# Optimization experiments

Measured on AMD Instinct MI355X. Metric: run time of the kernel, lower is better.

Reference implementation:

```python
import jax, jax.numpy as jnp
import numpy as np

B, D, N, P, MAXG, K = 1024, 128, 131072, 64, 2048, 16


def _l2norm(x, eps=1e-12):
    # matches torch F.normalize: x / clamp_min(||x||, eps)
    return x / jnp.maximum(jnp.linalg.norm(x, axis=-1, keepdims=True), eps)


def setup_inputs() -> dict:
    key = jax.random.key(0)
    ks = jax.random.split(key, 7)
    query = jax.random.normal(ks[0], (B, D), jnp.float32)
    keys = jax.random.normal(ks[1], (N, D), jnp.float32)
    vals = jax.random.normal(ks[2], (N, D), jnp.float32)
    labels = jax.random.normal(ks[3], (N,), jnp.float32)
    hard_assignment = jax.random.randint(ks[4], (B,), 0, P)
    cached_groups = jax.random.randint(ks[5], (P, MAXG), 0, N)
    group_sizes = jax.random.randint(ks[6], (P,), K, MAXG + 1)
    # -1 padding beyond each group's size, as in cache_sample_groups
    pos = jnp.arange(MAXG)[None, :]
    cached_groups = jnp.where(pos < group_sizes[:, None], cached_groups, -1)
    return dict(query=query, keys=keys, vals=vals, labels=labels,
                hard_assignment=hard_assignment, cached_groups=cached_groups,
                group_sizes=group_sizes, k=K)


def reference(query, keys, vals, labels, hard_assignment, cached_groups, group_sizes, k):
    n = keys.shape[0]
    q_norm = _l2norm(query)                                  # (B, D)
    grp = group_sizes[hard_assignment]                       # (B,)
    normal = grp >= k                                        # fallback mask (grp<k -> zeros)
    cand = cached_groups[hard_assignment]                    # (B, G) padded with -1
    valid = cand >= 0
    safe = jnp.clip(cand, 0, n - 1)
    keys_c = _l2norm(keys[safe])                             # (B, G, D) gathered + normalized
    sim = jnp.einsum('bd,bgd->bg', q_norm, keys_c)           # cosine similarity
    sim = jnp.where(valid, sim, -1e9)                        # mask padded candidates
    _, top = jax.lax.top_k(sim, k)                           # (B, k) positions within group
    i_final = jnp.take_along_axis(safe, top, axis=1)         # (B, k) memory-bank indices
    nk = keys[i_final]                                       # (B, k, D)
    nv = vals[i_final]                                       # (B, k, D)
    nl = labels[jnp.clip(i_final, 0, n - 1)]                 # (B, k)
    m = normal[:, None]
    nk = jnp.where(m[..., None], nk, 0.0)
    nv = jnp.where(m[..., None], nv, 0.0)
    nl = jnp.where(m, nl, 0.0)
    top_k_idx = jnp.where(m, i_final, 0)
    return nk, nv, nl, top_k_idx
```

## Files before the change

### kernel.cpp

```cpp
#include <hip/hip_runtime.h>

#define DIMS 128
#define KTOP 16
#define SMAX 2048
#define SLICE 64
#define CK 64
#define QT 32
#define CQ 32
#define NTHR 256

__device__ __forceinline__ unsigned long long packsim(float v, int g) {
    unsigned u = __float_as_uint(v);
    u = (u & 0x80000000u) ? ~u : (u | 0x80000000u);
    return ((unsigned long long)u << 32) | (unsigned)(0xFFFFFFFFu - (unsigned)g);
}

__global__ __launch_bounds__(1024)
void bucket_kernel(const int* __restrict__ hard_assign,
                   int* __restrict__ qcount, int* __restrict__ qlist, int B, int P)
{
    const int t = threadIdx.x;
    for (int i = t; i < P; i += 1024) qcount[i] = 0;
    __syncthreads();
    for (int b = t; b < B; b += 1024) {
        const int p = hard_assign[b];
        const int slot = atomicAdd(&qcount[p], 1);
        qlist[(size_t)p * B + slot] = b;
    }
}

__global__ __launch_bounds__(NTHR)
void score_kernel(const float* __restrict__ query,
                  const float* __restrict__ keys,
                  const int*   __restrict__ cached_groups,
                  const int*   __restrict__ qcount,
                  const int*   __restrict__ qlist,
                  float* __restrict__ sims,
                  int B, int N, int MAXG, int nslice)
{
    __shared__ float s_keyT[DIMS * CK];
    __shared__ float s_qT[DIMS * CQ];
    __shared__ float s_inv[SLICE];
    __shared__ int   s_g[SLICE];
    __shared__ int   s_qb[QT];

    const int p = blockIdx.x / nslice;
    const int s = blockIdx.x % nslice;
    const int cnt = qcount[p];
    if (cnt == 0) return;

    const int t = threadIdx.x;
    const int base = s * SLICE;
    const int* gp = cached_groups + (size_t)p * MAXG;
    const int* ql = qlist + (size_t)p * B;

    if (t < 128) {
        const int r    = t >> 1;
        const int half = t & 1;
        const int cand = (base + r < MAXG) ? gp[base + r] : -1;
        if (half == 0) s_g[r] = cand;
        const int sf = cand < 0 ? 0 : (cand > N - 1 ? N - 1 : cand);
        const float* kr = keys + (size_t)sf * DIMS + half * 64;
        float4 v[16];
        #pragma unroll
        for (int i = 0; i < 16; ++i)
            v[i] = *(const float4*)(kr + i * 4);
        float ks = 0.0f;
        #pragma unroll
        for (int i = 0; i < 16; ++i) {
            const int d = half * 64 + i * 4;
            ks += v[i].x * v[i].x + v[i].y * v[i].y
                + v[i].z * v[i].z + v[i].w * v[i].w;
            s_keyT[(d + 0) * CK + r] = v[i].x;
            s_keyT[(d + 1) * CK + r] = v[i].y;
            s_keyT[(d + 2) * CK + r] = v[i].z;
            s_keyT[(d + 3) * CK + r] = v[i].w;
        }
        ks += __shfl_xor(ks, 1, 64);
        if (half == 0) s_inv[r] = 1.0f / fmaxf(sqrtf(ks), 1e-12f);
    } else {
        const int tq   = t - 128;
        const int q    = tq & 31;
        const int dblk = tq >> 5;
        const int sq   = ql[(q < cnt) ? q : (cnt - 1)];
        if (dblk == 0) s_qb[q] = sq;
        const float* qr = query + (size_t)sq * DIMS + dblk * 32;
        #pragma unroll
        for (int i = 0; i < 8; ++i) {
            const float4 v = *(const float4*)(qr + i * 4);
            const int d = dblk * 32 + i * 4;
            s_qT[(d + 0) * CQ + q] = v.x;
            s_qT[(d + 1) * CQ + q] = v.y;
            s_qT[(d + 2) * CQ + q] = v.z;
            s_qT[(d + 3) * CQ + q] = v.w;
        }
    }
    __syncthreads();

    const int q0 = (t >> 4) * 2;
    const int c0 = (t & 15) * 4;

    for (int qbase = 0; ; ) {
        float acc[2][4];
        #pragma unroll
        for (int a = 0; a < 2; ++a)
            #pragma unroll
            for (int bb = 0; bb < 4; ++bb) acc[a][bb] = 0.0f;

        #pragma unroll 8
        for (int k = 0; k < DIMS; ++k) {
            const float2 aq = *(const float2*)&s_qT[k * CQ + q0];
            const float4 bk = *(const float4*)&s_keyT[k * CK + c0];
            acc[0][0] += aq.x * bk.x; acc[0][1] += aq.x * bk.y;
            acc[0][2] += aq.x * bk.z; acc[0][3] += aq.x * bk.w;
            acc[1][0] += aq.y * bk.x; acc[1][1] += aq.y * bk.y;
            acc[1][2] += aq.y * bk.z; acc[1][3] += aq.y * bk.w;
        }

        const float4 inv = *(const float4*)&s_inv[c0];
        const int4   gv  = *(const int4*)&s_g[c0];
        #pragma unroll
        for (int qi = 0; qi < 2; ++qi) {
            const int ii = qbase + q0 + qi;
            if (ii < cnt) {
                const int b = s_qb[q0 + qi];
                float4 o;
                o.x = (gv.x >= 0) ? acc[qi][0] * inv.x : -1.0e9f;
                o.y = (gv.y >= 0) ? acc[qi][1] * inv.y : -1.0e9f;
                o.z = (gv.z >= 0) ? acc[qi][2] * inv.z : -1.0e9f;
                o.w = (gv.w >= 0) ? acc[qi][3] * inv.w : -1.0e9f;
                float* dst = sims + (size_t)b * MAXG + base + c0;
                if (base + c0 + 3 < MAXG) {
                    *(float4*)dst = o;
                } else {
                    if (base + c0 + 0 < MAXG) dst[0] = o.x;
                    if (base + c0 + 1 < MAXG) dst[1] = o.y;
                    if (base + c0 + 2 < MAXG) dst[2] = o.z;
                }
            }
        }

        qbase += QT;
        if (qbase >= cnt) break;

        __syncthreads();
        if (t >= 128) {
            const int tq   = t - 128;
            const int q    = tq & 31;
            const int dblk = tq >> 5;
            const int ii   = qbase + q;
            const int sq   = ql[(ii < cnt) ? ii : (cnt - 1)];
            if (dblk == 0) s_qb[q] = sq;
            const float* qr = query + (size_t)sq * DIMS + dblk * 32;
            #pragma unroll
            for (int i = 0; i < 8; ++i) {
                const float4 v = *(const float4*)(qr + i * 4);
                const int d = dblk * 32 + i * 4;
                s_qT[(d + 0) * CQ + q] = v.x;
                s_qT[(d + 1) * CQ + q] = v.y;
                s_qT[(d + 2) * CQ + q] = v.z;
                s_qT[(d + 3) * CQ + q] = v.w;
            }
        }
        __syncthreads();
    }
}

#define CASW(x,y) { if ((x) < (y)) { const unsigned long long _t = (x); (x) = (y); (y) = _t; } }

__global__ __launch_bounds__(256)
void topk_gather_kernel(const float* __restrict__ keys,
                        const float* __restrict__ vals,
                        const float* __restrict__ labels,
                        const int*   __restrict__ hard_assign,
                        const int*   __restrict__ cached_groups,
                        const int*   __restrict__ group_sizes,
                        const float* __restrict__ sims,
                        float* __restrict__ out,
                        int B, int MAXG)
{
    const int b = blockIdx.x, t = threadIdx.x;
    const int lane = t & 63, w = t >> 6;
    const int sub = t & 15, cg = t >> 4;

    __shared__ unsigned long long s_merge[64];
    __shared__ int s_wing[KTOP];

    const int p = hard_assign[b];
    const int grpsz = group_sizes[p];
    const bool normal = (grpsz >= KTOP);
    const int* gptr = cached_groups + (size_t)p * MAXG;
    const float* simrow = sims + (size_t)b * MAXG;

    unsigned long long k0, k1, k2, k3, k4, k5, k6, k7;
    {
        const int g0 = w * (SMAX / 4) + lane * 8;
        if (g0 + 7 < MAXG) {
            const float4 va = *(const float4*)(simrow + g0);
            const float4 vb = *(const float4*)(simrow + g0 + 4);
            k0 = packsim(va.x, g0 + 0); k1 = packsim(va.y, g0 + 1);
            k2 = packsim(va.z, g0 + 2); k3 = packsim(va.w, g0 + 3);
            k4 = packsim(vb.x, g0 + 4); k5 = packsim(vb.y, g0 + 5);
            k6 = packsim(vb.z, g0 + 6); k7 = packsim(vb.w, g0 + 7);
        } else {
            #define LDK(j) packsim((g0 + (j) < MAXG) ? simrow[g0 + (j)] : -3.0e38f, g0 + (j))
            k0 = LDK(0); k1 = LDK(1); k2 = LDK(2); k3 = LDK(3);
            k4 = LDK(4); k5 = LDK(5); k6 = LDK(6); k7 = LDK(7);
            #undef LDK
        }
    }
    CASW(k0,k1) CASW(k2,k3) CASW(k4,k5) CASW(k6,k7)
    CASW(k0,k2) CASW(k1,k3) CASW(k4,k6) CASW(k5,k7)
    CASW(k1,k2) CASW(k5,k6)
    CASW(k0,k4) CASW(k1,k5) CASW(k2,k6) CASW(k3,k7)
    CASW(k2,k4) CASW(k3,k5)
    CASW(k1,k2) CASW(k3,k4) CASW(k5,k6)

    #pragma unroll 1
    for (int r = 0; r < KTOP; ++r) {
        unsigned long long wm = k0;
        #pragma unroll
        for (int off = 1; off < 64; off <<= 1) {
            const unsigned long long o = __shfl_xor(wm, off, 64);
            wm = (o > wm) ? o : wm;
        }
        if (lane == 0) s_merge[w * KTOP + r] = wm;
        if (k0 == wm) {
            k0 = k1; k1 = k2; k2 = k3; k3 = k4;
            k4 = k5; k5 = k6; k6 = k7; k7 = 0ull;
        }
    }
    __syncthreads();

    if (w == 0) {
        unsigned long long u = s_merge[lane];
        #pragma unroll
        for (int k = 2; k <= 64; k <<= 1) {
            #pragma unroll
            for (int j = k >> 1; j > 0; j >>= 1) {
                const unsigned long long o = __shfl_xor(u, j, 64);
                const bool low = (lane & j) == 0;
                const bool asc = (lane & k) == 0;
                const unsigned long long mn = (u < o) ? u : o;
                const unsigned long long mx = (u < o) ? o : u;
                u = (low == asc) ? mn : mx;
            }
        }
        if (lane >= 64 - KTOP)
            s_wing[63 - lane] = (int)(0xFFFFFFFFu - (unsigned)(u & 0xFFFFFFFFull));
    }
    __syncthreads();

    const int g    = s_wing[cg];
    const int cand = gptr[g];
    const int idx  = cand < 0 ? 0 : cand;

    const size_t BK = (size_t)B * KTOP;
    float* out_nk = out;
    float* out_nv = out + BK * DIMS;
    float* out_nl = out + 2 * BK * DIMS;
    float* out_id = out_nl + BK;

    const size_t od = ((size_t)b * KTOP + cg) * DIMS + sub * 8;
    if (normal) {
        const float* kr = keys + (size_t)idx * DIMS + sub * 8;
        const float* vr = vals + (size_t)idx * DIMS + sub * 8;
        *(float4*)(out_nk + od)     = *(const float4*)(kr);
        *(float4*)(out_nk + od + 4) = *(const float4*)(kr + 4);
        *(float4*)(out_nv + od)     = *(const float4*)(vr);
        *(float4*)(out_nv + od + 4) = *(const float4*)(vr + 4);
        if (sub == 0) {
            out_nl[(size_t)b * KTOP + cg] = labels[idx];
            out_id[(size_t)b * KTOP + cg] = (float)idx;
        }
    } else {
        const float4 z = make_float4(0.f, 0.f, 0.f, 0.f);
        *(float4*)(out_nk + od)     = z;
        *(float4*)(out_nk + od + 4) = z;
        *(float4*)(out_nv + od)     = z;
        *(float4*)(out_nv + od + 4) = z;
        if (sub == 0) {
            out_nl[(size_t)b * KTOP + cg] = 0.0f;
            out_id[(size_t)b * KTOP + cg] = 0.0f;
        }
    }
}

extern "C" void kernel_launch(void* const* d_in, const int* in_sizes, int n_in,
                              void* d_out, int out_size, void* d_ws, size_t ws_size,
                              hipStream_t stream) {
    const float* query  = (const float*)d_in[0];
    const float* keys   = (const float*)d_in[1];
    const float* vals   = (const float*)d_in[2];
    const float* labels = (const float*)d_in[3];
    const int* hard_assign   = (const int*)d_in[4];
    const int* cached_groups = (const int*)d_in[5];
    const int* group_sizes   = (const int*)d_in[6];

    const int B = in_sizes[0] / DIMS;
    const int N = in_sizes[1] / DIMS;
    const int P = in_sizes[6];
    const int MAXG = in_sizes[5] / P;
    const int nslice = (MAXG + SLICE - 1) / SLICE;

    float* sims  = (float*)d_ws;
    int* qcount  = (int*)((char*)d_ws + (size_t)B * MAXG * 4);
    int* qlist   = qcount + P;

    bucket_kernel<<<1, 1024, 0, stream>>>(hard_assign, qcount, qlist, B, P);

    score_kernel<<<P * nslice, NTHR, 0, stream>>>(
        query, keys, cached_groups, qcount, qlist, sims, B, N, MAXG, nslice);

    topk_gather_kernel<<<B, 256, 0, stream>>>(
        keys, vals, labels, hard_assign, cached_groups, group_sizes, sims,
        (float*)d_out, B, MAXG);
}
```

Before: 50.36 us.

## Process two key slices per block with register prefetch of second slice

```diff
diff --git a/kernel.cpp b/kernel.cpp
--- a/kernel.cpp
+++ b/kernel.cpp
@@ -36,7 +36,7 @@
                   const int*   __restrict__ qcount,
                   const int*   __restrict__ qlist,
                   float* __restrict__ sims,
-                  int B, int N, int MAXG, int nslice)
+                  int B, int N, int MAXG, int nslice, int npair)
 {
     __shared__ float s_keyT[DIMS * CK];
     __shared__ float s_qT[DIMS * CQ];
@@ -44,20 +44,28 @@
     __shared__ int   s_g[SLICE];
     __shared__ int   s_qb[QT];
 
-    const int p = blockIdx.x / nslice;
-    const int s = blockIdx.x % nslice;
+    const int p  = blockIdx.x / npair;
+    const int pr = blockIdx.x % npair;
+    const int s0 = pr * 2;
+    const int s1 = s0 + 1;
     const int cnt = qcount[p];
     if (cnt == 0) return;
 
     const int t = threadIdx.x;
-    const int base = s * SLICE;
+    const int base0 = s0 * SLICE;
+    const int base1 = s1 * SLICE;
+    const bool have1 = (s1 < nslice);
     const int* gp = cached_groups + (size_t)p * MAXG;
     const int* ql = qlist + (size_t)p * B;
 
+    const int r    = t >> 1;
+    const int half = t & 1;
+
+    int cand1 = -1;
+    if (t < 128 && have1 && base1 + r < MAXG) cand1 = gp[base1 + r];
+
     if (t < 128) {
-        const int r    = t >> 1;
-        const int half = t & 1;
-        const int cand = (base + r < MAXG) ? gp[base + r] : -1;
+        const int cand = (base0 + r < MAXG) ? gp[base0 + r] : -1;
         if (half == 0) s_g[r] = cand;
         const int sf = cand < 0 ? 0 : (cand > N - 1 ? N - 1 : cand);
         const float* kr = keys + (size_t)sf * DIMS + half * 64;
@@ -97,73 +105,128 @@
     }
     __syncthreads();
 
+    float4 pv[16];
+    {
+        const int sf1 = cand1 < 0 ? 0 : (cand1 > N - 1 ? N - 1 : cand1);
+        if (t < 128 && have1) {
+            const float* kr1 = keys + (size_t)sf1 * DIMS + half * 64;
+            #pragma unroll
+            for (int i = 0; i < 16; ++i)
+                pv[i] = *(const float4*)(kr1 + i * 4);
+        }
+    }
+    asm volatile("" ::: "memory");
+
     const int q0 = (t >> 4) * 2;
     const int c0 = (t & 15) * 4;
 
-    for (int qbase = 0; ; ) {
-        float acc[2][4];
-        #pragma unroll
-        for (int a = 0; a < 2; ++a)
+    auto compute_slice = [&](const int base) {
+        for (int qbase = 0; ; ) {
+            float acc[2][4];
             #pragma unroll
-            for (int bb = 0; bb < 4; ++bb) acc[a][bb] = 0.0f;
-
-        #pragma unroll 8
-        for (int k = 0; k < DIMS; ++k) {
-            const float2 aq = *(const float2*)&s_qT[k * CQ + q0];
-            const float4 bk = *(const float4*)&s_keyT[k * CK + c0];
-            acc[0][0] += aq.x * bk.x; acc[0][1] += aq.x * bk.y;
-            acc[0][2] += aq.x * bk.z; acc[0][3] += aq.x * bk.w;
-            acc[1][0] += aq.y * bk.x; acc[1][1] += aq.y * bk.y;
-            acc[1][2] += aq.y * bk.z; acc[1][3] += aq.y * bk.w;
-        }
-
-        const float4 inv = *(const float4*)&s_inv[c0];
-        const int4   gv  = *(const int4*)&s_g[c0];
-        #pragma unroll
-        for (int qi = 0; qi < 2; ++qi) {
-            const int ii = qbase + q0 + qi;
-            if (ii < cnt) {
-                const int b = s_qb[q0 + qi];
-                float4 o;
-                o.x = (gv.x >= 0) ? acc[qi][0] * inv.x : -1.0e9f;
-                o.y = (gv.y >= 0) ? acc[qi][1] * inv.y : -1.0e9f;
-                o.z = (gv.z >= 0) ? acc[qi][2] * inv.z : -1.0e9f;
-                o.w = (gv.w >= 0) ? acc[qi][3] * inv.w : -1.0e9f;
-                float* dst = sims + (size_t)b * MAXG + base + c0;
-                if (base + c0 + 3 < MAXG) {
-                    *(float4*)dst = o;
-                } else {
-                    if (base + c0 + 0 < MAXG) dst[0] = o.x;
-                    if (base + c0 + 1 < MAXG) dst[1] = o.y;
-                    if (base + c0 + 2 < MAXG) dst[2] = o.z;
+            for (int a = 0; a < 2; ++a)
+                #pragma unroll
+                for (int bb = 0; bb < 4; ++bb) acc[a][bb] = 0.0f;
+
+            #pragma unroll 8
+            for (int k = 0; k < DIMS; ++k) {
+                const float2 aq = *(const float2*)&s_qT[k * CQ + q0];
+                const float4 bk = *(const float4*)&s_keyT[k * CK + c0];
+                acc[0][0] += aq.x * bk.x; acc[0][1] += aq.x * bk.y;
+                acc[0][2] += aq.x * bk.z; acc[0][3] += aq.x * bk.w;
+                acc[1][0] += aq.y * bk.x; acc[1][1] += aq.y * bk.y;
+                acc[1][2] += aq.y * bk.z; acc[1][3] += aq.y * bk.w;
+            }
+
+            const float4 inv = *(const float4*)&s_inv[c0];
+            const int4   gv  = *(const int4*)&s_g[c0];
+            #pragma unroll
+            for (int qi = 0; qi < 2; ++qi) {
+                const int ii = qbase + q0 + qi;
+                if (ii < cnt) {
+                    const int b = s_qb[q0 + qi];
+                    float4 o;
+                    o.x = (gv.x >= 0) ? acc[qi][0] * inv.x : -1.0e9f;
+                    o.y = (gv.y >= 0) ? acc[qi][1] * inv.y : -1.0e9f;
+                    o.z = (gv.z >= 0) ? acc[qi][2] * inv.z : -1.0e9f;
+                    o.w = (gv.w >= 0) ? acc[qi][3] * inv.w : -1.0e9f;
+                    float* dst = sims + (size_t)b * MAXG + base + c0;
+                    if (base + c0 + 3 < MAXG) {
+                        *(float4*)dst = o;
+                    } else {
+                        if (base + c0 + 0 < MAXG) dst[0] = o.x;
+                        if (base + c0 + 1 < MAXG) dst[1] = o.y;
+                        if (base + c0 + 2 < MAXG) dst[2] = o.z;
+                    }
                 }
             }
-        }
-
-        qbase += QT;
-        if (qbase >= cnt) break;
-
-        __syncthreads();
-        if (t >= 128) {
-            const int tq   = t - 128;
-            const int q    = tq & 31;
-            const int dblk = tq >> 5;
-            const int ii   = qbase + q;
-            const int sq   = ql[(ii < cnt) ? ii : (cnt - 1)];
-            if (dblk == 0) s_qb[q] = sq;
-            const float* qr = query + (size_t)sq * DIMS + dblk * 32;
-            #pragma unroll
-            for (int i = 0; i < 8; ++i) {
-                const float4 v = *(const float4*)(qr + i * 4);
-                const int d = dblk * 32 + i * 4;
-                s_qT[(d + 0) * CQ + q] = v.x;
-                s_qT[(d + 1) * CQ + q] = v.y;
-                s_qT[(d + 2) * CQ + q] = v.z;
-                s_qT[(d + 3) * CQ + q] = v.w;
+
+            qbase += QT;
+            if (qbase >= cnt) break;
+
+            __syncthreads();
+            if (t >= 128) {
+                const int tq   = t - 128;
+                const int q    = tq & 31;
+                const int dblk = tq >> 5;
+                const int ii   = qbase + q;
+                const int sq   = ql[(ii < cnt) ? ii : (cnt - 1)];
+                if (dblk == 0) s_qb[q] = sq;
+                const float* qr = query + (size_t)sq * DIMS + dblk * 32;
+                #pragma unroll
+                for (int i = 0; i < 8; ++i) {
+                    const float4 v = *(const float4*)(qr + i * 4);
+                    const int d = dblk * 32 + i * 4;
+                    s_qT[(d + 0) * CQ + q] = v.x;
+                    s_qT[(d + 1) * CQ + q] = v.y;
+                    s_qT[(d + 2) * CQ + q] = v.z;
+                    s_qT[(d + 3) * CQ + q] = v.w;
+                }
             }
-        }
-        __syncthreads();
-    }
+            __syncthreads();
+        }
+    };
+
+    compute_slice(base0);
+
+    if (!have1) return;
+    __syncthreads();
+
+    if (t < 128) {
+        if (half == 0) s_g[r] = cand1;
+        float ks = 0.0f;
+        #pragma unroll
+        for (int i = 0; i < 16; ++i) {
+            const int d = half * 64 + i * 4;
+            ks += pv[i].x * pv[i].x + pv[i].y * pv[i].y
+                + pv[i].z * pv[i].z + pv[i].w * pv[i].w;
+            s_keyT[(d + 0) * CK + r] = pv[i].x;
+            s_keyT[(d + 1) * CK + r] = pv[i].y;
+            s_keyT[(d + 2) * CK + r] = pv[i].z;
+            s_keyT[(d + 3) * CK + r] = pv[i].w;
+        }
+        ks += __shfl_xor(ks, 1, 64);
+        if (half == 0) s_inv[r] = 1.0f / fmaxf(sqrtf(ks), 1e-12f);
+    } else if (cnt > QT) {
+        const int tq   = t - 128;
+        const int q    = tq & 31;
+        const int dblk = tq >> 5;
+        const int sq   = ql[(q < cnt) ? q : (cnt - 1)];
+        if (dblk == 0) s_qb[q] = sq;
+        const float* qr = query + (size_t)sq * DIMS + dblk * 32;
+        #pragma unroll
+        for (int i = 0; i < 8; ++i) {
+            const float4 v = *(const float4*)(qr + i * 4);
+            const int d = dblk * 32 + i * 4;
+            s_qT[(d + 0) * CQ + q] = v.x;
+            s_qT[(d + 1) * CQ + q] = v.y;
+            s_qT[(d + 2) * CQ + q] = v.z;
+            s_qT[(d + 3) * CQ + q] = v.w;
+        }
+    }
+    __syncthreads();
+
+    compute_slice(base1);
 }
 
 #define CASW(x,y) { if ((x) < (y)) { const unsigned long long _t = (x); (x) = (y); (y) = _t; } }
@@ -302,6 +365,7 @@
     const int P = in_sizes[6];
     const int MAXG = in_sizes[5] / P;
     const int nslice = (MAXG + SLICE - 1) / SLICE;
+    const int npair  = (nslice + 1) / 2;
 
     float* sims  = (float*)d_ws;
     int* qcount  = (int*)((char*)d_ws + (size_t)B * MAXG * 4);
@@ -309,8 +373,8 @@
 
     bucket_kernel<<<1, 1024, 0, stream>>>(hard_assign, qcount, qlist, B, P);
 
-    score_kernel<<<P * nslice, NTHR, 0, stream>>>(
-        query, keys, cached_groups, qcount, qlist, sims, B, N, MAXG, nslice);
+    score_kernel<<<P * npair, NTHR, 0, stream>>>(
+        query, keys, cached_groups, qcount, qlist, sims, B, N, MAXG, nslice, npair);
 
     topk_gather_kernel<<<B, 256, 0, stream>>>(
         keys, vals, labels, hard_assign, cached_groups, group_sizes, sims,
```

Result: slower. 52.08 us (+3.4%).
